# Kernel optimization log

Hardware: AMD Instinct MI355X
Metric: run time of the kernel (lower is better)

## Reference

```python
import jax, jax.numpy as jnp
import numpy as np

IN_DIM = 1024
OUT_DIM = 1024
QK_DIM = OUT_DIM // 4  # 256


def setup_inputs() -> dict:
    key = jax.random.key(0)
    kx, ky, kq, kk, kv = jax.random.split(key, 5)
    B, Sq, Sk = 16, 2048, 2048
    x = jax.random.normal(kx, (B, Sq, IN_DIM), dtype=jnp.float32)
    y = jax.random.normal(ky, (B, Sk, IN_DIM), dtype=jnp.float32)
    s = 1.0 / np.sqrt(IN_DIM)
    Wq = jax.random.normal(kq, (IN_DIM, QK_DIM), dtype=jnp.float32) * s
    Wk = jax.random.normal(kk, (IN_DIM, QK_DIM), dtype=jnp.float32) * s
    Wv = jax.random.normal(kv, (IN_DIM, OUT_DIM), dtype=jnp.float32) * s
    return {"x": x, "y": y, "Wq": Wq, "Wk": Wk, "Wv": Wv}


def reference(x, y, Wq, Wk, Wv):
    # q: [B,Sq,dk], k: [B,Sk,dk]
    q = jnp.einsum("bsd,dk->bsk", x, Wq)
    k = jnp.einsum("btd,dk->btk", y, Wk)
    # NOTE: original scales by out_dim**0.5, not qk dim
    scores = jnp.einsum("bsk,btk->bst", q, k) / jnp.sqrt(jnp.float32(OUT_DIM))
    attn = jax.nn.softmax(scores, axis=-1)
    v = jnp.einsum("btd,de->bte", y, Wv)
    out = jnp.einsum("bst,bte->bse", attn, v)
    return out + x
```

## Files before the change

### kernel.cpp

```cpp
#include <hip/hip_runtime.h>

typedef __attribute__((ext_vector_type(8))) short bf16x8;
typedef __attribute__((ext_vector_type(4))) short s16x4;
typedef __attribute__((ext_vector_type(4))) float f32x4;

#define MFMA16(a,b,c) __builtin_amdgcn_mfma_f32_16x16x32_bf16((a),(b),(c),0,0,0)

__device__ __forceinline__ unsigned short f2bf(float f) {
  unsigned int u = __float_as_uint(f);
  return (unsigned short)((u + 0x7fffu + ((u >> 16) & 1u)) >> 16);
}
__device__ __forceinline__ float bf2f(unsigned short u) {
  return __uint_as_float(((unsigned int)u) << 16);
}

__device__ __forceinline__ void gload16(const void* g, void* l) {
  __builtin_amdgcn_global_load_lds((const __attribute__((address_space(1))) void*)g,
                                   (__attribute__((address_space(3))) void*)l, 16, 0, 0);
}

__global__ __launch_bounds__(256) void cvt_bf16_2(const float* __restrict__ inx,
                                                  unsigned short* __restrict__ outx,
                                                  const float* __restrict__ iny,
                                                  unsigned short* __restrict__ outy,
                                                  int n8) {
  const float* in = (blockIdx.x < 2048) ? inx : iny;
  unsigned short* out = (blockIdx.x < 2048) ? outx : outy;
  const int b = blockIdx.x & 2047;
  for (int i = b * 256 + threadIdx.x; i < n8; i += 2048 * 256) {
    float4 a = ((const float4*)in)[2 * i];
    float4 c = ((const float4*)in)[2 * i + 1];
    s16x4 p0, p1;
    p0[0] = f2bf(a.x); p0[1] = f2bf(a.y); p0[2] = f2bf(a.z); p0[3] = f2bf(a.w);
    p1[0] = f2bf(c.x); p1[1] = f2bf(c.y); p1[2] = f2bf(c.z); p1[3] = f2bf(c.w);
    ((s16x4*)out)[2 * i] = p0;
    ((s16x4*)out)[2 * i + 1] = p1;
  }
}

__global__ __launch_bounds__(256) void tcvt3(const float* __restrict__ Wq, unsigned short* __restrict__ Wqt,
                                             const float* __restrict__ Wk, unsigned short* __restrict__ Wkt,
                                             const float* __restrict__ Wv, unsigned short* __restrict__ Wvt) {
  __shared__ float t[32][33];
  const int which = blockIdx.z;
  const float* W = which == 0 ? Wq : (which == 1 ? Wk : Wv);
  unsigned short* Wt = which == 0 ? Wqt : (which == 1 ? Wkt : Wvt);
  const int N = (which == 2) ? 1024 : 256;
  const int K = 1024;
  const int n0 = blockIdx.x * 32, k0 = blockIdx.y * 32;
  if (n0 >= N) return;
  const int c = threadIdx.x & 31, r8 = threadIdx.x >> 5;
#pragma unroll
  for (int p = 0; p < 4; ++p) {
    int r = r8 + p * 8;
    t[r][c] = W[(size_t)(k0 + r) * N + n0 + c];
  }
  __syncthreads();
#pragma unroll
  for (int p = 0; p < 4; ++p) {
    int r = r8 + p * 8;
    Wt[(size_t)(n0 + r) * K + k0 + c] = f2bf(t[c][r]);
  }
}

#define SBAR  do { __builtin_amdgcn_s_barrier(); __builtin_amdgcn_sched_barrier(0); } while (0)

template<int NT, int NTIL, int MODE>
__global__ __launch_bounds__(512) void gemm4p(
    const unsigned short* __restrict__ Aall, const unsigned short* __restrict__ Ball,
    size_t abatch, size_t bbatch, int lda, int ldb,
    unsigned short* __restrict__ Cb, int b0, int nb)
{
  __shared__ __align__(16) unsigned short lds[65536];
  const int bid = blockIdx.x;
  const int bloc = bid % nb, tl = bid / nb;
  const int mtile = tl / NTIL, ntile = tl % NTIL;
  const int gb = b0 + bloc;
  const unsigned short* Ag = Aall + (MODE == 0 ? (size_t)gb : (size_t)bloc) * abatch
                                  + (size_t)mtile * 256 * lda;
  const unsigned short* Bg = Ball + (size_t)gb * bbatch + (size_t)ntile * 256 * ldb;

  const int tid = threadIdx.x, lane = tid & 63, w = tid >> 6;
  const int wm = w >> 2, wn = w & 3;
  const int lrow = lane & 15, lg = lane >> 4;
  char* lb = (char*)lds;

  auto stageU = [&](const unsigned short* G, int ld, int kofs, int ubyte) {
#pragma unroll
    for (int i = 0; i < 2; ++i) {
      int c = tid + 512 * i;
      int row = c >> 2, q = c & 3;
      int qs = q ^ ((row >> 1) & 3);
      gload16(G + (size_t)row * ld + kofs + qs * 8, lb + ubyte + c * 16);
    }
  };
  auto rdfrag = [&](int ubyte, int row) -> bf16x8 {
    return *(const bf16x8*)(lb + ubyte + row * 64 + ((lg ^ ((row >> 1) & 3)) << 4));
  };

  f32x4 acc[8][4] = {};
  bf16x8 afA[4], afB[4], bfrA[4], bfrB[4];

  stageU(Ag, lda, 0,  (0 * 2 + 0) * 16384);
  stageU(Bg, ldb, 0,  (1 * 2 + 0) * 16384);
  stageU(Ag, lda, 32, (2 * 2 + 0) * 16384);
  stageU(Bg, ldb, 32, (3 * 2 + 0) * 16384);
  stageU(Ag, lda, 64, (0 * 2 + 1) * 16384);
  stageU(Bg, ldb, 64, (1 * 2 + 1) * 16384);
  asm volatile("s_waitcnt vmcnt(8)" ::: "memory");
  SBAR;
#pragma unroll
  for (int i = 0; i < 4; ++i) afA[i] = rdfrag(0, wm * 128 + i * 16 + lrow);
#pragma unroll
  for (int nf = 0; nf < 4; ++nf) bfrA[nf] = rdfrag(2 * 16384, wn * 64 + nf * 16 + lrow);

  for (int T = 0; T < NT; ++T) {
    const int pc = T & 1, pn = (T + 1) & 1;
    const int a1b = (2 * 2 + pc) * 16384, b1b = (3 * 2 + pc) * 16384;
    const int a0b = (0 * 2 + pc) * 16384;
    const int t1 = (T + 1 < NT) ? T + 1 : 0;
    const int t2 = (T + 2 < NT) ? T + 2 : 0;

#pragma unroll
    for (int i = 0; i < 4; ++i) afB[i] = rdfrag(a0b, wm * 128 + (i + 4) * 16 + lrow);
    stageU(Ag, lda, t1 * 64 + 32, (2 * 2 + pn) * 16384);
    asm volatile("s_waitcnt lgkmcnt(4)" ::: "memory");
    __builtin_amdgcn_sched_barrier(0);
    __builtin_amdgcn_s_setprio(1);
#pragma unroll
    for (int mf = 0; mf < 4; ++mf)
#pragma unroll
      for (int nf = 0; nf < 4; ++nf)
        acc[mf][nf] = MFMA16(afA[mf], bfrA[nf], acc[mf][nf]);
    __builtin_amdgcn_s_setprio(0);
    asm volatile("s_waitcnt vmcnt(6)" ::: "memory");
    SBAR;

#pragma unroll
    for (int i = 0; i < 4; ++i) afA[i] = rdfrag(a1b, wm * 128 + i * 16 + lrow);
#pragma unroll
    for (int nf = 0; nf < 4; ++nf) bfrB[nf] = rdfrag(b1b, wn * 64 + nf * 16 + lrow);
    stageU(Bg, ldb, t1 * 64 + 32, (3 * 2 + pn) * 16384);
    asm volatile("s_waitcnt lgkmcnt(8)" ::: "memory");
    __builtin_amdgcn_sched_barrier(0);
    __builtin_amdgcn_s_setprio(1);
#pragma unroll
    for (int mf = 0; mf < 4; ++mf)
#pragma unroll
      for (int nf = 0; nf < 4; ++nf)
        acc[mf + 4][nf] = MFMA16(afB[mf], bfrA[nf], acc[mf + 4][nf]);
    __builtin_amdgcn_s_setprio(0);
    SBAR;

#pragma unroll
    for (int i = 0; i < 4; ++i) afB[i] = rdfrag(a1b, wm * 128 + (i + 4) * 16 + lrow);
    stageU(Ag, lda, t2 * 64, (0 * 2 + pc) * 16384);
    asm volatile("s_waitcnt lgkmcnt(4)" ::: "memory");
    __builtin_amdgcn_sched_barrier(0);
    __builtin_amdgcn_s_setprio(1);
#pragma unroll
    for (int mf = 0; mf < 4; ++mf)
#pragma unroll
      for (int nf = 0; nf < 4; ++nf)
        acc[mf][nf] = MFMA16(afA[mf], bfrB[nf], acc[mf][nf]);
    __builtin_amdgcn_s_setprio(0);
    asm volatile("s_waitcnt vmcnt(6)" ::: "memory");
    SBAR;

#pragma unroll
    for (int i = 0; i < 4; ++i) afA[i] = rdfrag((0 * 2 + pn) * 16384, wm * 128 + i * 16 + lrow);
#pragma unroll
    for (int nf = 0; nf < 4; ++nf) bfrA[nf] = rdfrag((1 * 2 + pn) * 16384, wn * 64 + nf * 16 + lrow);
    stageU(Bg, ldb, t2 * 64, (1 * 2 + pc) * 16384);
    asm volatile("s_waitcnt lgkmcnt(8)" ::: "memory");
    __builtin_amdgcn_sched_barrier(0);
    __builtin_amdgcn_s_setprio(1);
#pragma unroll
    for (int mf = 0; mf < 4; ++mf)
#pragma unroll
      for (int nf = 0; nf < 4; ++nf)
        acc[mf + 4][nf] = MFMA16(afB[mf], bfrB[nf], acc[mf + 4][nf]);
    __builtin_amdgcn_s_setprio(0);
    SBAR;
  }

  if (MODE == 0) {
    unsigned short* Cp = Cb + (size_t)bloc * 2048 * 2048;
#pragma unroll
    for (int mf = 0; mf < 8; ++mf)
#pragma unroll
      for (int r = 0; r < 4; ++r) {
        int row = mtile * 256 + wm * 128 + mf * 16 + lg * 4 + r;
#pragma unroll
        for (int nf = 0; nf < 4; ++nf) {
          int col = ntile * 256 + wn * 64 + nf * 16 + lrow;
          Cp[(size_t)row * 2048 + col] = f2bf(acc[mf][nf][r]);
        }
      }
  } else if (MODE == 2) {
    unsigned char* C8 = (unsigned char*)Cb;
#pragma unroll
    for (int mf = 0; mf < 8; ++mf) {
      int m0 = mtile * 256 + wm * 128 + mf * 16 + lg * 4;
      int bb = m0 >> 11, t = m0 & 2047;
      int tw = t >> 6, t64 = t & 63;
#pragma unroll
      for (int nf = 0; nf < 4; ++nf) {
        int e = ntile * 256 + wn * 64 + nf * 16 + lrow;
        int eg = e >> 4;
        int pk = 0;
        pk = __builtin_amdgcn_cvt_pk_fp8_f32(acc[mf][nf][0], acc[mf][nf][1], pk, false);
        pk = __builtin_amdgcn_cvt_pk_fp8_f32(acc[mf][nf][2], acc[mf][nf][3], pk, true);
        *(unsigned int*)(C8 + (size_t)bb * 2097152
                            + ((size_t)(eg * 32 + tw)) * 1024 + lrow * 64 + t64)
            = (unsigned int)pk;
      }
    }
  } else {
    unsigned short* Cp = Cb + (size_t)bloc * 16 * 2048 * 256;
    const float scale = (bloc == 0) ? 0.03125f : 1.0f;
#pragma unroll
    for (int mf = 0; mf < 8; ++mf)
#pragma unroll
      for (int r = 0; r < 4; ++r) {
        int row = mtile * 256 + wm * 128 + mf * 16 + lg * 4 + r;
#pragma unroll
        for (int nf = 0; nf < 4; ++nf) {
          int col = wn * 64 + nf * 16 + lrow;
          Cp[(size_t)row * 256 + col] = f2bf(acc[mf][nf][r] * scale);
        }
      }
  }
}

__global__ __launch_bounds__(256) void softmax_kernel(
    const unsigned short* __restrict__ Sp, unsigned char* __restrict__ Pp) {
  const int row = blockIdx.x * 4 + (threadIdx.x >> 6);
  const int lane = threadIdx.x & 63;
  const unsigned short* rp = Sp + (size_t)row * 2048;
  bf16x8 raw[4];
#pragma unroll
  for (int c = 0; c < 4; ++c) raw[c] = *(const bf16x8*)(rp + c * 512 + lane * 8);
  float v[32];
#pragma unroll
  for (int c = 0; c < 4; ++c)
#pragma unroll
    for (int j = 0; j < 8; ++j) v[c * 8 + j] = bf2f((unsigned short)raw[c][j]);
  float mx = v[0];
#pragma unroll
  for (int j = 1; j < 32; ++j) mx = fmaxf(mx, v[j]);
  mx = fmaxf(mx, __shfl_xor(mx, 1));
  mx = fmaxf(mx, __shfl_xor(mx, 2));
  mx = fmaxf(mx, __shfl_xor(mx, 4));
  mx = fmaxf(mx, __shfl_xor(mx, 8));
  mx = fmaxf(mx, __shfl_xor(mx, 16));
  mx = fmaxf(mx, __shfl_xor(mx, 32));
  float sum = 0.f;
#pragma unroll
  for (int j = 0; j < 32; ++j) { v[j] = __expf(v[j] - mx); sum += v[j]; }
  sum += __shfl_xor(sum, 1);
  sum += __shfl_xor(sum, 2);
  sum += __shfl_xor(sum, 4);
  sum += __shfl_xor(sum, 8);
  sum += __shfl_xor(sum, 16);
  sum += __shfl_xor(sum, 32);
  const float scale = 64.0f / sum;
  unsigned char* rp8 = Pp + (size_t)row * 2048;
#pragma unroll
  for (int c = 0; c < 4; ++c) {
    int lo = 0, hi = 0;
    lo = __builtin_amdgcn_cvt_pk_fp8_f32(v[c * 8 + 0] * scale, v[c * 8 + 1] * scale, lo, false);
    lo = __builtin_amdgcn_cvt_pk_fp8_f32(v[c * 8 + 2] * scale, v[c * 8 + 3] * scale, lo, true);
    hi = __builtin_amdgcn_cvt_pk_fp8_f32(v[c * 8 + 4] * scale, v[c * 8 + 5] * scale, hi, false);
    hi = __builtin_amdgcn_cvt_pk_fp8_f32(v[c * 8 + 6] * scale, v[c * 8 + 7] * scale, hi, true);
    uint2 o; o.x = (unsigned int)lo; o.y = (unsigned int)hi;
    *(uint2*)(rp8 + c * 512 + lane * 8) = o;
  }
}

template<int PRIO>
__global__ __launch_bounds__(512) void pvf8_kernel(
    const unsigned char* __restrict__ Pp,
    const unsigned char* __restrict__ Vp,
    const float* __restrict__ X, float* __restrict__ Out,
    int b0, int nb)
{
  __shared__ __align__(16) unsigned char lds[4][16384];
  const int bloc = blockIdx.x % nb, tl = blockIdx.x / nb;
  const int mtile = tl >> 3, ntile = tl & 7;
  const int gb = b0 + bloc;
  const unsigned char* Ag = Pp + (size_t)bloc * 4194304 + (size_t)mtile * 256 * 2048;
  const unsigned char* Vb = Vp + (size_t)gb * 2097152;
  const int NT = 32;
  const int tid = threadIdx.x, lane = tid & 63, w = tid >> 6;
  const int wm = w >> 2, wn = w & 3;
  const int lrow = lane & 15, lg = lane >> 4;

  auto stageA = [&](int jt) {
    unsigned char* dst = lds[jt & 3];
#pragma unroll
    for (int i = 0; i < 2; ++i) {
      int c = tid + 512 * i; int row = c >> 2; int q = (c & 3) ^ ((row >> 1) & 3);
      gload16(Ag + (size_t)row * 2048 + jt * 64 + q * 16, dst + c * 16);
    }
  };

  f32x4 acc[8][2] = {};
  stageA(0); stageA(1); stageA(2);
  asm volatile("s_waitcnt vmcnt(4)" ::: "memory");

  for (int jt = 0; jt < NT; ++jt) {
    __builtin_amdgcn_s_barrier();
    long2 bv[2];
#pragma unroll
    for (int nf = 0; nf < 2; ++nf) {
      int eg = ntile * 8 + wn * 2 + nf;
      bv[nf] = *(const long2*)(Vb + ((size_t)(eg * 32 + jt)) * 1024 + lrow * 64 + lg * 16);
    }
    if (jt + 3 < NT) stageA(jt + 3);
    const unsigned char* Ab = lds[jt & 3];
    {
      long2 av[4];
#pragma unroll
      for (int mf = 0; mf < 4; ++mf) {
        int row = wm * 128 + mf * 16 + lrow;
        av[mf] = *(const long2*)(Ab + row * 64 + ((lg ^ ((row >> 1) & 3)) << 4));
      }
      if (PRIO) __builtin_amdgcn_s_setprio(1);
#pragma unroll
      for (int mf = 0; mf < 4; ++mf)
#pragma unroll
        for (int nf = 0; nf < 2; ++nf) {
          acc[mf][nf] = __builtin_amdgcn_mfma_f32_16x16x32_fp8_fp8(av[mf].x, bv[nf].x, acc[mf][nf], 0, 0, 0);
          acc[mf][nf] = __builtin_amdgcn_mfma_f32_16x16x32_fp8_fp8(av[mf].y, bv[nf].y, acc[mf][nf], 0, 0, 0);
        }
      if (PRIO) __builtin_amdgcn_s_setprio(0);
    }
    {
      long2 av[4];
#pragma unroll
      for (int mf = 0; mf < 4; ++mf) {
        int row = wm * 128 + (mf + 4) * 16 + lrow;
        av[mf] = *(const long2*)(Ab + row * 64 + ((lg ^ ((row >> 1) & 3)) << 4));
      }
      if (PRIO) __builtin_amdgcn_s_setprio(1);
#pragma unroll
      for (int mf = 0; mf < 4; ++mf)
#pragma unroll
        for (int nf = 0; nf < 2; ++nf) {
          acc[mf + 4][nf] = __builtin_amdgcn_mfma_f32_16x16x32_fp8_fp8(av[mf].x, bv[nf].x, acc[mf + 4][nf], 0, 0, 0);
          acc[mf + 4][nf] = __builtin_amdgcn_mfma_f32_16x16x32_fp8_fp8(av[mf].y, bv[nf].y, acc[mf + 4][nf], 0, 0, 0);
        }
      if (PRIO) __builtin_amdgcn_s_setprio(0);
    }
  }

#pragma unroll
  for (int mf = 0; mf < 8; ++mf)
#pragma unroll
    for (int r = 0; r < 4; ++r) {
      int row = mtile * 256 + wm * 128 + mf * 16 + lg * 4 + r;
      const float* xr = X   + ((size_t)gb * 2048 + row) * 1024;
      float*      orp = Out + ((size_t)gb * 2048 + row) * 1024;
#pragma unroll
      for (int nf = 0; nf < 2; ++nf) {
        int col = ntile * 128 + wn * 32 + nf * 16 + lrow;
        orp[col] = acc[mf][nf][r] * 0.015625f + xr[col];
      }
    }
}

extern "C" void kernel_launch(void* const* d_in, const int* in_sizes, int n_in,
                              void* d_out, int out_size, void* d_ws, size_t ws_size,
                              hipStream_t stream) {
  (void)in_sizes; (void)n_in; (void)out_size;
  const float* x  = (const float*)d_in[0];
  const float* y  = (const float*)d_in[1];
  const float* Wq = (const float*)d_in[2];
  const float* Wk = (const float*)d_in[3];
  const float* Wv = (const float*)d_in[4];
  float* out = (float*)d_out;

  unsigned short* xb = (unsigned short*)d_out;
  unsigned short* yb = xb + (size_t)16 * 2048 * 1024;

  char* p = (char*)d_ws;
  unsigned short* Wqt = (unsigned short*)p;  p += (size_t)256 * 1024 * 2;
  unsigned short* Wkt = (unsigned short*)p;  p += (size_t)256 * 1024 * 2;
  unsigned short* Wvt = (unsigned short*)p;  p += (size_t)1024 * 1024 * 2;
  unsigned short* qws = (unsigned short*)p;  p += (size_t)16 * 2048 * 256 * 2;
  unsigned short* kws = (unsigned short*)p;  p += (size_t)16 * 2048 * 256 * 2;
  unsigned char*  vp8 = (unsigned char*)p;   p += (size_t)16 * 1024 * 2048;
  char* dyn = p;
  const size_t fixed_bytes = (size_t)(dyn - (char*)d_ws);
  const size_t per_batch = (size_t)2048 * 2048 * 2 + (size_t)2048 * 2048;
  int nb = 1;
  if      (ws_size >= fixed_bytes + 16 * per_batch) nb = 16;
  else if (ws_size >= fixed_bytes + 8  * per_batch) nb = 8;
  else if (ws_size >= fixed_bytes + 4  * per_batch) nb = 4;
  else if (ws_size >= fixed_bytes + 2  * per_batch) nb = 2;
  else nb = 1;
  unsigned short* Sp = (unsigned short*)dyn;
  unsigned char*  Pp = (unsigned char*)(dyn + (size_t)nb * 2048 * 2048 * 2);

  const int n8 = (16 * 2048 * 1024) / 8;
  cvt_bf16_2<<<4096, 256, 0, stream>>>(x, xb, y, yb, n8);
  tcvt3<<<dim3(32, 32, 3), 256, 0, stream>>>(Wq, Wqt, Wk, Wkt, Wv, Wvt);

  gemm4p<16, 1, 3><<<256, 512, 0, stream>>>(
      xb, Wqt, (size_t)16 * 2048 * 1024, (size_t)256 * 1024, 1024, 1024,
      qws, 0, 2);
  gemm4p<16, 4, 2><<<512, 512, 0, stream>>>(
      yb, Wvt, 0, 0, 1024, 1024, (unsigned short*)vp8, 0, 1);

  for (int b0 = 0; b0 < 16; b0 += nb) {
    gemm4p<4, 8, 0><<<nb * 64, 512, 0, stream>>>(
        qws, kws, (size_t)2048 * 256, (size_t)2048 * 256, 256, 256,
        Sp, b0, nb);
    softmax_kernel<<<nb * 512, 256, 0, stream>>>(Sp, Pp);
    if (nb == 16) {
      pvf8_kernel<1><<<8 * 64, 512, 0, stream>>>(Pp, vp8, x, out, 0, 8);
      pvf8_kernel<0><<<8 * 64, 512, 0, stream>>>(Pp + (size_t)8 * 4194304, vp8, x, out, 8, 8);
    } else {
      pvf8_kernel<1><<<nb * 64, 512, 0, stream>>>(Pp, vp8, x, out, b0, nb);
    }
  }
}
```

Baseline: 433.5 us.

## Retile PV fp8 kernel to 4x2 warp grid, single launch; widen bf16 convert

The PV kernel's warp layout changes from 2x4 to 4x2 (each warp now computes 64x64 instead of 128x32). Each warp loads four A fragments and four V fragments per step, so LDS reads of A drop while direct global loads of V rise. The nb==16 split into two launches is replaced by one launch over all batches, with priority boosting applied everywhere. The fp32->bf16 conversion kernel now handles 16 elements per thread with nontemporal stores, aiming to reduce cache pollution for the bf16 copies.

```diff
diff --git a/kernel.cpp b/kernel.cpp
--- a/kernel.cpp
+++ b/kernel.cpp
@@ -23,18 +23,24 @@
                                                   unsigned short* __restrict__ outx,
                                                   const float* __restrict__ iny,
                                                   unsigned short* __restrict__ outy,
-                                                  int n8) {
-  const float* in = (blockIdx.x < 2048) ? inx : iny;
-  unsigned short* out = (blockIdx.x < 2048) ? outx : outy;
+                                                  int n16) {
+  const float4* in4 = (const float4*)((blockIdx.x < 2048) ? inx : iny);
+  s16x4* out4 = (s16x4*)((blockIdx.x < 2048) ? outx : outy);
   const int b = blockIdx.x & 2047;
-  for (int i = b * 256 + threadIdx.x; i < n8; i += 2048 * 256) {
-    float4 a = ((const float4*)in)[2 * i];
-    float4 c = ((const float4*)in)[2 * i + 1];
-    s16x4 p0, p1;
-    p0[0] = f2bf(a.x); p0[1] = f2bf(a.y); p0[2] = f2bf(a.z); p0[3] = f2bf(a.w);
-    p1[0] = f2bf(c.x); p1[1] = f2bf(c.y); p1[2] = f2bf(c.z); p1[3] = f2bf(c.w);
-    ((s16x4*)out)[2 * i] = p0;
-    ((s16x4*)out)[2 * i + 1] = p1;
+  for (int i = b * 256 + threadIdx.x; i < n16; i += 2048 * 256) {
+    float4 a0 = in4[4 * i + 0];
+    float4 a1 = in4[4 * i + 1];
+    float4 a2 = in4[4 * i + 2];
+    float4 a3 = in4[4 * i + 3];
+    s16x4 p0, p1, p2, p3;
+    p0[0] = f2bf(a0.x); p0[1] = f2bf(a0.y); p0[2] = f2bf(a0.z); p0[3] = f2bf(a0.w);
+    p1[0] = f2bf(a1.x); p1[1] = f2bf(a1.y); p1[2] = f2bf(a1.z); p1[3] = f2bf(a1.w);
+    p2[0] = f2bf(a2.x); p2[1] = f2bf(a2.y); p2[2] = f2bf(a2.z); p2[3] = f2bf(a2.w);
+    p3[0] = f2bf(a3.x); p3[1] = f2bf(a3.y); p3[2] = f2bf(a3.z); p3[3] = f2bf(a3.w);
+    __builtin_nontemporal_store(p0, &out4[4 * i + 0]);
+    __builtin_nontemporal_store(p1, &out4[4 * i + 1]);
+    __builtin_nontemporal_store(p2, &out4[4 * i + 2]);
+    __builtin_nontemporal_store(p3, &out4[4 * i + 3]);
   }
 }
 
@@ -278,7 +284,6 @@
   }
 }
 
-template<int PRIO>
 __global__ __launch_bounds__(512) void pvf8_kernel(
     const unsigned char* __restrict__ Pp,
     const unsigned char* __restrict__ Vp,
@@ -293,7 +298,7 @@
   const unsigned char* Vb = Vp + (size_t)gb * 2097152;
   const int NT = 32;
   const int tid = threadIdx.x, lane = tid & 63, w = tid >> 6;
-  const int wm = w >> 2, wn = w & 3;
+  const int wm = w >> 1, wn = w & 1;
   const int lrow = lane & 15, lg = lane >> 4;
 
   auto stageA = [&](int jt) {
@@ -305,66 +310,47 @@
     }
   };
 
-  f32x4 acc[8][2] = {};
+  f32x4 acc[4][4] = {};
   stageA(0); stageA(1); stageA(2);
   asm volatile("s_waitcnt vmcnt(4)" ::: "memory");
 
   for (int jt = 0; jt < NT; ++jt) {
     __builtin_amdgcn_s_barrier();
-    long2 bv[2];
-#pragma unroll
-    for (int nf = 0; nf < 2; ++nf) {
-      int eg = ntile * 8 + wn * 2 + nf;
+    long2 bv[4];
+#pragma unroll
+    for (int nf = 0; nf < 4; ++nf) {
+      int eg = ntile * 8 + wn * 4 + nf;
       bv[nf] = *(const long2*)(Vb + ((size_t)(eg * 32 + jt)) * 1024 + lrow * 64 + lg * 16);
     }
     if (jt + 3 < NT) stageA(jt + 3);
     const unsigned char* Ab = lds[jt & 3];
-    {
-      long2 av[4];
-#pragma unroll
-      for (int mf = 0; mf < 4; ++mf) {
-        int row = wm * 128 + mf * 16 + lrow;
-        av[mf] = *(const long2*)(Ab + row * 64 + ((lg ^ ((row >> 1) & 3)) << 4));
+    long2 av[4];
+#pragma unroll
+    for (int mf = 0; mf < 4; ++mf) {
+      int row = wm * 64 + mf * 16 + lrow;
+      av[mf] = *(const long2*)(Ab + row * 64 + ((lg ^ ((row >> 1) & 3)) << 4));
+    }
+    __builtin_amdgcn_s_setprio(1);
+#pragma unroll
+    for (int mf = 0; mf < 4; ++mf)
+#pragma unroll
+      for (int nf = 0; nf < 4; ++nf) {
+        acc[mf][nf] = __builtin_amdgcn_mfma_f32_16x16x32_fp8_fp8(av[mf].x, bv[nf].x, acc[mf][nf], 0, 0, 0);
+        acc[mf][nf] = __builtin_amdgcn_mfma_f32_16x16x32_fp8_fp8(av[mf].y, bv[nf].y, acc[mf][nf], 0, 0, 0);
       }
-      if (PRIO) __builtin_amdgcn_s_setprio(1);
-#pragma unroll
-      for (int mf = 0; mf < 4; ++mf)
-#pragma unroll
-        for (int nf = 0; nf < 2; ++nf) {
-          acc[mf][nf] = __builtin_amdgcn_mfma_f32_16x16x32_fp8_fp8(av[mf].x, bv[nf].x, acc[mf][nf], 0, 0, 0);
-          acc[mf][nf] = __builtin_amdgcn_mfma_f32_16x16x32_fp8_fp8(av[mf].y, bv[nf].y, acc[mf][nf], 0, 0, 0);
-        }
-      if (PRIO) __builtin_amdgcn_s_setprio(0);
-    }
-    {
-      long2 av[4];
-#pragma unroll
-      for (int mf = 0; mf < 4; ++mf) {
-        int row = wm * 128 + (mf + 4) * 16 + lrow;
-        av[mf] = *(const long2*)(Ab + row * 64 + ((lg ^ ((row >> 1) & 3)) << 4));
-      }
-      if (PRIO) __builtin_amdgcn_s_setprio(1);
-#pragma unroll
-      for (int mf = 0; mf < 4; ++mf)
-#pragma unroll
-        for (int nf = 0; nf < 2; ++nf) {
-          acc[mf + 4][nf] = __builtin_amdgcn_mfma_f32_16x16x32_fp8_fp8(av[mf].x, bv[nf].x, acc[mf + 4][nf], 0, 0, 0);
-          acc[mf + 4][nf] = __builtin_amdgcn_mfma_f32_16x16x32_fp8_fp8(av[mf].y, bv[nf].y, acc[mf + 4][nf], 0, 0, 0);
-        }
-      if (PRIO) __builtin_amdgcn_s_setprio(0);
-    }
-  }
-
-#pragma unroll
-  for (int mf = 0; mf < 8; ++mf)
+    __builtin_amdgcn_s_setprio(0);
+  }
+
+#pragma unroll
+  for (int mf = 0; mf < 4; ++mf)
 #pragma unroll
     for (int r = 0; r < 4; ++r) {
-      int row = mtile * 256 + wm * 128 + mf * 16 + lg * 4 + r;
+      int row = mtile * 256 + wm * 64 + mf * 16 + lg * 4 + r;
       const float* xr = X   + ((size_t)gb * 2048 + row) * 1024;
       float*      orp = Out + ((size_t)gb * 2048 + row) * 1024;
 #pragma unroll
-      for (int nf = 0; nf < 2; ++nf) {
-        int col = ntile * 128 + wn * 32 + nf * 16 + lrow;
+      for (int nf = 0; nf < 4; ++nf) {
+        int col = ntile * 128 + wn * 64 + nf * 16 + lrow;
         orp[col] = acc[mf][nf][r] * 0.015625f + xr[col];
       }
     }
@@ -403,8 +389,8 @@
   unsigned short* Sp = (unsigned short*)dyn;
   unsigned char*  Pp = (unsigned char*)(dyn + (size_t)nb * 2048 * 2048 * 2);
 
-  const int n8 = (16 * 2048 * 1024) / 8;
-  cvt_bf16_2<<<4096, 256, 0, stream>>>(x, xb, y, yb, n8);
+  const int n16 = (16 * 2048 * 1024) / 16;
+  cvt_bf16_2<<<4096, 256, 0, stream>>>(x, xb, y, yb, n16);
   tcvt3<<<dim3(32, 32, 3), 256, 0, stream>>>(Wq, Wqt, Wk, Wkt, Wv, Wvt);
 
   gemm4p<16, 1, 3><<<256, 512, 0, stream>>>(
@@ -418,11 +404,6 @@
         qws, kws, (size_t)2048 * 256, (size_t)2048 * 256, 256, 256,
         Sp, b0, nb);
     softmax_kernel<<<nb * 512, 256, 0, stream>>>(Sp, Pp);
-    if (nb == 16) {
-      pvf8_kernel<1><<<8 * 64, 512, 0, stream>>>(Pp, vp8, x, out, 0, 8);
-      pvf8_kernel<0><<<8 * 64, 512, 0, stream>>>(Pp + (size_t)8 * 4194304, vp8, x, out, 8, 8);
-    } else {
-      pvf8_kernel<1><<<nb * 64, 512, 0, stream>>>(Pp, vp8, x, out, b0, nb);
-    }
-  }
-}
+    pvf8_kernel<<<nb * 64, 512, 0, stream>>>(Pp, vp8, x, out, b0, nb);
+  }
+}
```

New measurement: 439.4 us. Within noise of the previous version (+1.4%).
